# Kernel tuning notes

Measured on AMD Instinct MI355X. Metric: run time of the kernel, lower is better.

## Reference

```python
import jax, jax.numpy as jnp
import numpy as np

N, E, F, S, R, H = 10000, 160000, 128, 10, 8, 64
SH_OFF = [0, 1, 4, 9]
SH_DIM = [1, 3, 5, 7]
AVG_NUM_NEIGHBORS = 16.0


def setup_inputs() -> dict:
    key = jax.random.key(0)
    ks = jax.random.split(key, 16)
    species = jax.random.randint(ks[0], (N,), 0, S)
    node_attrs = jax.nn.one_hot(species, S, dtype=jnp.float32)
    node_feats = jax.random.normal(ks[1], (N, F), dtype=jnp.float32)
    edge_attrs = jax.random.normal(ks[2], (E, 16), dtype=jnp.float32)
    edge_feats = jax.random.normal(ks[3], (E, R), dtype=jnp.float32)
    edge_index = jax.random.randint(ks[4], (2, E), 0, N)
    # learned parameters
    W_skip_node = jax.random.normal(ks[5], (F, S, F), dtype=jnp.float32)
    W_up = jax.random.normal(ks[6], (F, F), dtype=jnp.float32)
    mlp_w1 = jax.random.normal(ks[7], (R, H), dtype=jnp.float32)
    mlp_w2 = jax.random.normal(ks[8], (H, H), dtype=jnp.float32)
    mlp_w3 = jax.random.normal(ks[9], (H, H), dtype=jnp.float32)
    mlp_w4 = jax.random.normal(ks[10], (H, 4 * F), dtype=jnp.float32)  # conv_tp.weight_numel = 512
    W_lin = jax.random.normal(ks[11], (4, F, F), dtype=jnp.float32)
    W_skip_msg = jax.random.normal(ks[12], (4, F, S, F), dtype=jnp.float32)
    W_out = jax.random.normal(ks[13], (F, F), dtype=jnp.float32)
    return dict(node_attrs=node_attrs, node_feats=node_feats, edge_attrs=edge_attrs,
                edge_feats=edge_feats, edge_index=edge_index, species=species,
                W_skip_node=W_skip_node, W_up=W_up, mlp_w1=mlp_w1, mlp_w2=mlp_w2,
                mlp_w3=mlp_w3, mlp_w4=mlp_w4, W_lin=W_lin, W_skip_msg=W_skip_msg,
                W_out=W_out)


def reference(node_attrs, node_feats, edge_attrs, edge_feats, edge_index, species,
              W_skip_node, W_up, mlp_w1, mlp_w2, mlp_w3, mlp_w4,
              W_lin, W_skip_msg, W_out):
    sender, receiver = edge_index[0], edge_index[1]
    num_nodes = node_feats.shape[0]
    num_edges = edge_attrs.shape[0]

    # skip_tp_node: FullyConnectedTensorProduct(128x0e, 10x0e -> 128x0e), fan_in = 128*10
    skip = jnp.einsum('nu,nv,uvw->nw', node_feats, node_attrs, W_skip_node) * (1.0 / np.sqrt(F * S))

    # linear_up: 128x0e -> 128x0e
    h = (node_feats @ W_up) * (1.0 / np.sqrt(F))

    # radial MLP (e3nn FullyConnectedNet: no bias, w/sqrt(fan_in), silu on hidden layers)
    t = edge_feats
    for W in (mlp_w1, mlp_w2, mlp_w3):
        t = jax.nn.silu((t @ W) * (1.0 / np.sqrt(W.shape[0])))
    tp_w = (t @ mlp_w4) * (1.0 / np.sqrt(H))  # [E, 512]

    # conv_tp (gather -> 0e x l -> l 'uvu' TP) fused with scatter_sum per l-block
    hs = h[sender]  # [E, 128]
    msgs = []
    for l in range(4):
        d = SH_DIM[l]
        w_l = tp_w[:, l * F:(l + 1) * F]                       # [E, 128]
        sh_l = edge_attrs[:, SH_OFF[l]:SH_OFF[l] + d]          # [E, d]
        mji = (hs * w_l)[:, :, None] * sh_l[:, None, :]        # [E, 128, d]
        m = jax.ops.segment_sum(mji.reshape(num_edges, F * d), receiver,
                                num_segments=num_nodes)
        msgs.append(m.reshape(num_nodes, F, d))

    inv_avg = 1.0 / np.sqrt(AVG_NUM_NEIGHBORS)
    # linear (per-l 128->128) / sqrt(avg_num_neighbors), then skip_tp_msg (x 10x0e attrs)
    blocks = []
    for l in range(4):
        x = jnp.einsum('num,uw->nwm', msgs[l], W_lin[l]) * (inv_avg / np.sqrt(F))
        x = jnp.einsum('num,nv,uvw->nwm', x, node_attrs, W_skip_msg[l]) * (1.0 / np.sqrt(F * S))
        blocks.append(x)

    # linear_out: target -> 128x0e keeps only the scalar (l=0) block
    message = (blocks[0][:, :, 0] @ W_out) * (1.0 / np.sqrt(F))  # [N, 128]
    return message, skip
```

## Files before the change

kernel.cpp:

```cpp
#include <hip/hip_runtime.h>
#include <math.h>

#define NFEAT 128
#define NSPEC 10

__global__ void k_histboth(const int* __restrict__ species, const int* __restrict__ edge_index,
                           int* __restrict__ counts, int* __restrict__ ehist, int N, int E) {
    int i = blockIdx.x * blockDim.x + threadIdx.x;
    if (i < N) atomicAdd(&counts[species[i]], 1);
    if (i < E) atomicAdd(&ehist[edge_index[E + i]], 1);
}

__global__ void k_build(const int* __restrict__ counts, int* __restrict__ cursor,
                        int4* __restrict__ table, int* __restrict__ nTiles) {
    __shared__ int off[NSPEC + 1], ts[NSPEC + 1], cnt[NSPEC];
    const int t = threadIdx.x;
    if (t == 0) {
        int o = 0, tt = 0;
        for (int s = 0; s < NSPEC; s++) {
            cnt[s] = counts[s];
            off[s] = o; ts[s] = tt;
            o += cnt[s]; tt += (cnt[s] + 63) >> 6;
        }
        off[NSPEC] = o; ts[NSPEC] = tt;
        nTiles[0] = tt;
    }
    __syncthreads();
    if (t < NSPEC) cursor[t] = off[t];
    int nt = ts[NSPEC];
    for (int i = t; i < nt; i += blockDim.x) {
        int s = 0;
        while (ts[s + 1] <= i) s++;
        int b = i - ts[s];
        table[i] = make_int4(s, off[s] + b * 64, min(64, cnt[s] - b * 64), 0);
    }
}

__global__ void k_scatter(const int* __restrict__ species, int* __restrict__ cursor,
                          int* __restrict__ sorted, int N) {
    int i = blockIdx.x * blockDim.x + threadIdx.x;
    if (i < N) {
        int p = atomicAdd(&cursor[species[i]], 1);
        sorted[p] = i;
    }
}

__global__ void k_escan(const int* __restrict__ ehist, int* __restrict__ ecursor, int N) {
    __shared__ int ssum[256];
    const int t = threadIdx.x;
    const int chunk = (N + 255) / 256;
    const int lo = t * chunk;
    const int hi = min(lo + chunk, N);
    int local = 0;
    for (int i = lo; i < hi; i++) local += ehist[i];
    ssum[t] = local;
    __syncthreads();
    for (int off = 1; off < 256; off <<= 1) {
        int x = (t >= off) ? ssum[t - off] : 0;
        __syncthreads();
        ssum[t] += x;
        __syncthreads();
    }
    int run = ssum[t] - local;
    for (int i = lo; i < hi; i++) {
        ecursor[i] = run;
        run += ehist[i];
    }
}

__global__ void k_egather(const int* __restrict__ edge_index, const float* __restrict__ edge_attrs,
                          const float* __restrict__ edge_feats, int* __restrict__ ecursor,
                          int* __restrict__ sendG, int* __restrict__ recvG,
                          float* __restrict__ sh0G, float* __restrict__ efG, int E) {
    int i = blockIdx.x * blockDim.x + threadIdx.x;
    if (i < E) {
        int r = edge_index[E + i];
        int p = atomicAdd(&ecursor[r], 1);
        sendG[p] = edge_index[i];
        recvG[p] = r;
        sh0G[p]  = edge_attrs[(long)i * 16];
        float4 v0 = *(const float4*)(edge_feats + (long)i * 8);
        float4 v1 = *(const float4*)(edge_feats + (long)i * 8 + 4);
        *(float4*)(efG + (long)p * 8)     = v0;
        *(float4*)(efG + (long)p * 8 + 4) = v1;
    }
}

template <int BC>
__global__ __launch_bounds__(256) void k_gemm(
    const float* __restrict__ A, int aStride,
    const float* __restrict__ B, int bStride, int bSpecStride,
    float* __restrict__ C, int cStride, int cChunkY,
    int M, float alpha,
    const int* __restrict__ sorted,
    const int4* __restrict__ table,
    const int* __restrict__ nTiles)
{
    __shared__ float At[128][64];
    __shared__ float Bs[128][BC];
    const int t = threadIdx.x;
    const int gy = blockIdx.y;

    int start, cnt, spec = 0;
    if (table) {
        if (blockIdx.x >= nTiles[0]) return;
        int4 te = table[blockIdx.x];
        spec = te.x; start = te.y; cnt = te.z;
    } else {
        start = blockIdx.x * 64;
        cnt = M - start;
        if (cnt <= 0) return;
        if (cnt > 64) cnt = 64;
    }

    {
        const float* Bp = B + (long)spec * bSpecStride + (long)gy * BC;
        constexpr int F4R = BC / 4;
        #pragma unroll
        for (int i = 0; i < (128 * F4R) / 256; i++) {
            int idx = t + 256 * i;
            int k = idx / F4R;
            int c = (idx % F4R) * 4;
            *(float4*)&Bs[k][c] = *(const float4*)(Bp + (long)k * bStride + c);
        }
    }
    {
        int r = t & 63;
        int kc = (t >> 6) * 32;
        if (r < cnt) {
            int grow = table ? sorted[start + r] : (start + r);
            const float4* src = (const float4*)(A + (long)grow * aStride + kc);
            #pragma unroll
            for (int i = 0; i < 8; i++) {
                float4 v = src[i];
                At[kc + 4*i + 0][r] = v.x;
                At[kc + 4*i + 1][r] = v.y;
                At[kc + 4*i + 2][r] = v.z;
                At[kc + 4*i + 3][r] = v.w;
            }
        } else {
            #pragma unroll
            for (int i = 0; i < 32; i++) At[kc + i][r] = 0.0f;
        }
    }
    __syncthreads();

    constexpr int CG   = BC / 4;
    constexpr int ROWS = BC / 16;
    const int c0 = (t % CG) * 4;
    const int r0 = (t / CG) * ROWS;
    float acc[ROWS][4] = {};
    #pragma unroll 8
    for (int k = 0; k < 128; k++) {
        float4 b = *(const float4*)&Bs[k][c0];
        float av[ROWS];
        #pragma unroll
        for (int i = 0; i < ROWS / 4; i++) {
            float4 a = *(const float4*)&At[k][r0 + 4 * i];
            av[4*i + 0] = a.x; av[4*i + 1] = a.y; av[4*i + 2] = a.z; av[4*i + 3] = a.w;
        }
        #pragma unroll
        for (int i = 0; i < ROWS; i++) {
            acc[i][0] += av[i] * b.x;
            acc[i][1] += av[i] * b.y;
            acc[i][2] += av[i] * b.z;
            acc[i][3] += av[i] * b.w;
        }
    }
    #pragma unroll
    for (int i = 0; i < ROWS; i++) {
        int r = r0 + i;
        if (r < cnt) {
            int grow = table ? sorted[start + r] : (start + r);
            float4 v = make_float4(acc[i][0] * alpha, acc[i][1] * alpha,
                                   acc[i][2] * alpha, acc[i][3] * alpha);
            *(float4*)&C[(long)gy * cChunkY + (long)grow * cStride + c0] = v;
        }
    }
}

__global__ __launch_bounds__(256) void k_hs(
    const float* __restrict__ A,
    const float* __restrict__ Wup,
    const float* __restrict__ Wsn,
    float* __restrict__ h, float* __restrict__ skip,
    const int* __restrict__ sorted, const int4* __restrict__ table,
    const int* __restrict__ nTiles, float aH, float aSkip)
{
    __shared__ float At[128][64];
    __shared__ float Bs[128][64];
    const int t = threadIdx.x;
    const int gy = blockIdx.y;
    if (blockIdx.x >= nTiles[0]) return;
    int4 te = table[blockIdx.x];
    const int spec = te.x, start = te.y, cnt = te.z;

    {
        int r = t & 63, kc = (t >> 6) * 32;
        if (r < cnt) {
            int grow = sorted[start + r];
            const float4* src = (const float4*)(A + (long)grow * NFEAT + kc);
            #pragma unroll
            for (int i = 0; i < 8; i++) {
                float4 v = src[i];
                At[kc + 4*i + 0][r] = v.x;
                At[kc + 4*i + 1][r] = v.y;
                At[kc + 4*i + 2][r] = v.z;
                At[kc + 4*i + 3][r] = v.w;
            }
        } else {
            #pragma unroll
            for (int i = 0; i < 32; i++) At[kc + i][r] = 0.0f;
        }
    }
    const int c0 = (t & 15) * 4;
    const int r0 = (t >> 4) * 4;
    #pragma unroll
    for (int pass = 0; pass < 2; pass++) {
        {
            const float* Bp = pass == 0 ? (Wup + gy * 64)
                                        : (Wsn + spec * NFEAT + gy * 64);
            const int bStride = pass == 0 ? NFEAT : NFEAT * NSPEC;
            #pragma unroll
            for (int i = 0; i < 8; i++) {
                int idx = t + 256 * i;
                int k = idx >> 4;
                int c = (idx & 15) * 4;
                *(float4*)&Bs[k][c] = *(const float4*)(Bp + (long)k * bStride + c);
            }
        }
        __syncthreads();
        float acc[4][4] = {};
        #pragma unroll 8
        for (int k = 0; k < 128; k++) {
            float4 b = *(const float4*)&Bs[k][c0];
            float4 a = *(const float4*)&At[k][r0];
            float av[4] = {a.x, a.y, a.z, a.w};
            #pragma unroll
            for (int i = 0; i < 4; i++) {
                acc[i][0] += av[i] * b.x;
                acc[i][1] += av[i] * b.y;
                acc[i][2] += av[i] * b.z;
                acc[i][3] += av[i] * b.w;
            }
        }
        float* dst   = pass == 0 ? h : skip;
        float  alpha = pass == 0 ? aH : aSkip;
        #pragma unroll
        for (int i = 0; i < 4; i++) {
            int r = r0 + i;
            if (r < cnt) {
                int grow = sorted[start + r];
                float4 v = make_float4(acc[i][0] * alpha, acc[i][1] * alpha,
                                       acc[i][2] * alpha, acc[i][3] * alpha);
                *(float4*)&dst[(long)grow * NFEAT + gy * 64 + c0] = v;
            }
        }
        __syncthreads();
    }
}

#define ASTR 20

__global__ __launch_bounds__(256, 5) void k_edge(
    const int*   __restrict__ sendG,
    const int*   __restrict__ recvG,
    const float* __restrict__ sh0G,
    const float* __restrict__ efG,
    const float* __restrict__ W1,
    const float* __restrict__ W2,
    const float* __restrict__ W3,
    const float* __restrict__ W4,
    const float* __restrict__ h,
    float*       __restrict__ msgs0,
    int E)
{
    __shared__ float W1s[8][64];
    __shared__ float actS[4][64 * ASTR];
    __shared__ float efS[4][8 * 16];
    __shared__ int   sendS[4][16];
    __shared__ int   recvS[4][16];
    __shared__ float sh0S[4][16];

    const int t = threadIdx.x;
    if (t < 128) ((float4*)W1s)[t] = ((const float4*)W1)[t];
    __syncthreads();

    const int wid = t >> 6, lane = t & 63;
    const int ntiles = (E + 15) >> 4;
    const int tile = blockIdx.x * 4 + wid;
    if (tile >= ntiles) return;
    const int base = tile << 4;

    float* act = actS[wid];
    float* ef  = efS[wid];

    {
        int g = lane & 15, p = base + g;
        bool ok = p < E;
        if (lane < 16)      sendS[wid][g] = ok ? sendG[p] : 0;
        else if (lane < 32) recvS[wid][g] = ok ? recvG[p] : -1;
        else if (lane < 48) sh0S[wid][g]  = ok ? sh0G[p]  : 0.0f;
    }
    {
        int idx = lane * 2, e = idx >> 3, k = idx & 7;
        int p = base + e;
        float2 v = make_float2(0.f, 0.f);
        if (p < E) v = *(const float2*)(efG + (long)p * 8 + k);
        ef[k * 16 + e]       = v.x;
        ef[(k + 1) * 16 + e] = v.y;
    }

    const float s1 = 0.3535533905932738f;
    const float s2 = 0.125f;
    const int e4 = lane & 3;
    const int j4 = lane >> 2;

    {
        float acc[4][4] = {};
        #pragma unroll
        for (int k = 0; k < 8; k++) {
            float4 a = *(const float4*)&ef[k * 16 + e4 * 4];
            float4 b = *(const float4*)&W1s[k][j4 * 4];
            float av[4] = {a.x, a.y, a.z, a.w};
            float bv[4] = {b.x, b.y, b.z, b.w};
            #pragma unroll
            for (int jj = 0; jj < 4; jj++)
                #pragma unroll
                for (int ee = 0; ee < 4; ee++)
                    acc[jj][ee] += av[ee] * bv[jj];
        }
        #pragma unroll
        for (int jj = 0; jj < 4; jj++) {
            float4 v; float x;
            x = acc[jj][0] * s1; v.x = x / (1.0f + __expf(-x));
            x = acc[jj][1] * s1; v.y = x / (1.0f + __expf(-x));
            x = acc[jj][2] * s1; v.z = x / (1.0f + __expf(-x));
            x = acc[jj][3] * s1; v.w = x / (1.0f + __expf(-x));
            *(float4*)&act[(j4 * 4 + jj) * ASTR + e4 * 4] = v;
        }
    }

    {
        float acc[4][4] = {};
        const float4* W2v = (const float4*)W2;
        #pragma unroll 4
        for (int k = 0; k < 64; k++) {
            float4 a = *(const float4*)&act[k * ASTR + e4 * 4];
            float4 b = W2v[k * 16 + j4];
            float av[4] = {a.x, a.y, a.z, a.w};
            float bv[4] = {b.x, b.y, b.z, b.w};
            #pragma unroll
            for (int jj = 0; jj < 4; jj++)
                #pragma unroll
                for (int ee = 0; ee < 4; ee++)
                    acc[jj][ee] += av[ee] * bv[jj];
        }
        #pragma unroll
        for (int jj = 0; jj < 4; jj++) {
            float4 v; float x;
            x = acc[jj][0] * s2; v.x = x / (1.0f + __expf(-x));
            x = acc[jj][1] * s2; v.y = x / (1.0f + __expf(-x));
            x = acc[jj][2] * s2; v.z = x / (1.0f + __expf(-x));
            x = acc[jj][3] * s2; v.w = x / (1.0f + __expf(-x));
            *(float4*)&act[(j4 * 4 + jj) * ASTR + e4 * 4] = v;
        }
    }

    {
        float acc[4][4] = {};
        const float4* W3v = (const float4*)W3;
        #pragma unroll 4
        for (int k = 0; k < 64; k++) {
            float4 a = *(const float4*)&act[k * ASTR + e4 * 4];
            float4 b = W3v[k * 16 + j4];
            float av[4] = {a.x, a.y, a.z, a.w};
            float bv[4] = {b.x, b.y, b.z, b.w};
            #pragma unroll
            for (int jj = 0; jj < 4; jj++)
                #pragma unroll
                for (int ee = 0; ee < 4; ee++)
                    acc[jj][ee] += av[ee] * bv[jj];
        }
        #pragma unroll
        for (int jj = 0; jj < 4; jj++) {
            float4 v; float x;
            x = acc[jj][0] * s2; v.x = x / (1.0f + __expf(-x));
            x = acc[jj][1] * s2; v.y = x / (1.0f + __expf(-x));
            x = acc[jj][2] * s2; v.z = x / (1.0f + __expf(-x));
            x = acc[jj][3] * s2; v.w = x / (1.0f + __expf(-x));
            *(float4*)&act[(j4 * 4 + jj) * ASTR + e4 * 4] = v;
        }
    }

    {
        const int c0 = lane * 2;
        float wacc[16][2] = {};
        #pragma unroll 4
        for (int k = 0; k < 64; k++) {
            float2 w4 = *(const float2*)&W4[k * 512 + c0];
            float4 a0 = *(const float4*)&act[k * ASTR + 0];
            float4 a1 = *(const float4*)&act[k * ASTR + 4];
            float4 a2 = *(const float4*)&act[k * ASTR + 8];
            float4 a3 = *(const float4*)&act[k * ASTR + 12];
            float av[16] = {a0.x, a0.y, a0.z, a0.w, a1.x, a1.y, a1.z, a1.w,
                            a2.x, a2.y, a2.z, a2.w, a3.x, a3.y, a3.z, a3.w};
            #pragma unroll
            for (int e = 0; e < 16; e++) {
                wacc[e][0] += av[e] * w4.x;
                wacc[e][1] += av[e] * w4.y;
            }
        }
        int cur = recvS[wid][0];
        float sum0 = 0.f, sum1 = 0.f;
        #pragma unroll
        for (int e = 0; e < 16; e++) {
            int rcv = recvS[wid][e];
            if (rcv != cur) {
                if (cur >= 0) {
                    atomicAdd(&msgs0[(long)cur * NFEAT + c0],     sum0);
                    atomicAdd(&msgs0[(long)cur * NFEAT + c0 + 1], sum1);
                }
                cur = rcv; sum0 = 0.f; sum1 = 0.f;
            }
            float f = sh0S[wid][e] * s2;
            int snd = sendS[wid][e];
            float2 hv = *(const float2*)&h[(long)snd * NFEAT + c0];
            sum0 += wacc[e][0] * f * hv.x;
            sum1 += wacc[e][1] * f * hv.y;
        }
        if (cur >= 0) {
            atomicAdd(&msgs0[(long)cur * NFEAT + c0],     sum0);
            atomicAdd(&msgs0[(long)cur * NFEAT + c0 + 1], sum1);
        }
    }
}

extern "C" void kernel_launch(void* const* d_in, const int* in_sizes, int n_in,
                              void* d_out, int out_size, void* d_ws, size_t ws_size,
                              hipStream_t stream) {
    const float* node_feats = (const float*)d_in[1];
    const float* edge_attrs = (const float*)d_in[2];
    const float* edge_feats = (const float*)d_in[3];
    const int*   edge_index = (const int*)  d_in[4];
    const int*   species    = (const int*)  d_in[5];
    const float* Wsn        = (const float*)d_in[6];
    const float* Wup        = (const float*)d_in[7];
    const float* W1         = (const float*)d_in[8];
    const float* W2         = (const float*)d_in[9];
    const float* W3         = (const float*)d_in[10];
    const float* W4         = (const float*)d_in[11];
    const float* Wlin       = (const float*)d_in[12];
    const float* Wsm        = (const float*)d_in[13];
    const float* Wout       = (const float*)d_in[14];

    const int N = in_sizes[5];
    const int E = in_sizes[4] / 2;
    const int NF = NFEAT;

    float* out     = (float*)d_out;
    float* message = out;
    float* skip    = out + (long)N * NF;

    char* wsb = (char*)d_ws;
    size_t off = 0;
    auto carve = [&](size_t bytes) { void* p = wsb + off; off = (off + bytes + 255) & ~(size_t)255; return p; };
    float* h      = (float*)carve((size_t)N * NF * 4);
    float* msgs0  = (float*)carve((size_t)N * NF * 4);
    float* Tst    = (float*)carve((size_t)NSPEC * NF * NF * 4);
    float* Comb   = (float*)carve((size_t)NSPEC * NF * NF * 4);
    int*   sorted = (int*)carve((size_t)N * 4);
    int*   counts = (int*)carve(64);
    int*   cursor = (int*)carve(64);
    int*   nTiles = (int*)carve(16);
    int4*  table  = (int4*)carve(256 * 16);
    int*   ehist  = (int*)carve((size_t)N * 4);
    int*   ecursor= (int*)carve((size_t)N * 4);
    int*   sendG  = (int*)carve((size_t)E * 4);
    int*   recvG  = (int*)carve((size_t)E * 4);
    float* sh0G   = (float*)carve((size_t)E * 4);
    float* efG    = (float*)carve((size_t)E * 8 * 4);

    const float aH    = 1.0f / sqrtf((float)NF);
    const float aSkip = 1.0f / sqrtf((float)(NF * NSPEC));
    const float cTot  = 0.25f / ((float)NF * sqrtf((float)(NF * NSPEC)));

    hipMemsetAsync(counts, 0, 64, stream);
    hipMemsetAsync(ehist, 0, (size_t)N * 4, stream);
    hipMemsetAsync(msgs0, 0, (size_t)N * NF * 4, stream);

    k_histboth<<<(max(N, E) + 255) / 256, 256, 0, stream>>>(species, edge_index, counts, ehist, N, E);
    k_build  <<<1, 256, 0, stream>>>(counts, cursor, table, nTiles);
    k_scatter<<<(N + 255) / 256, 256, 0, stream>>>(species, cursor, sorted, N);
    k_escan  <<<1, 256, 0, stream>>>(ehist, ecursor, N);
    k_egather<<<(E + 255) / 256, 256, 0, stream>>>(edge_index, edge_attrs, edge_feats,
                                                   ecursor, sendG, recvG, sh0G, efG, E);

    const int mTiles   = (N + 63) / 64;
    const int maxTiles = mTiles + NSPEC;

    k_hs<<<dim3(maxTiles, 2), 256, 0, stream>>>(
        node_feats, Wup, Wsn, h, skip, sorted, table, nTiles, aH, aSkip);

    k_gemm<128><<<dim3(2, NSPEC), 256, 0, stream>>>(
        Wlin, NF, Wsm, NF * NSPEC, 0, Tst, NF, NF * NF, NF, 1.0f, nullptr, nullptr, nullptr);

    k_gemm<128><<<dim3((NSPEC * NF) / 64, 1), 256, 0, stream>>>(
        Tst, NF, Wout, NF, 0, Comb, NF, NF, NSPEC * NF, cTot, nullptr, nullptr, nullptr);

    int eTiles = (E + 15) / 16;
    int eBlocks = (eTiles + 3) / 4;
    k_edge<<<eBlocks, 256, 0, stream>>>(
        sendG, recvG, sh0G, efG, W1, W2, W3, W4, h, msgs0, E);

    k_gemm<64><<<dim3(maxTiles, 2), 256, 0, stream>>>(
        msgs0, NF, Comb, NF, NF * NF, message, NF, 64, N, 1.0f, sorted, table, nTiles);
}
```

Baseline: 362.9 us.

## Compute radial MLP per edge in registers with one thread per edge

The edge kernel is restructured so each thread owns one edge and runs the whole radial MLP in registers. Weight reads are wave-uniform, so they can become scalar loads, which removes the shared-memory activation tiles and the cross-lane GEMM tiling. Blocks shrink to a single 64-lane wave covering 64 edges. The gather/scatter phase now stages the 128 used TP weights through shared memory in four 32-column chunks, with 32 lanes walking edges serially. This trades high register pressure and a half-idle, longer serial scatter loop for cheaper MLP arithmetic.

```diff
diff --git a/kernel.cpp b/kernel.cpp
--- a/kernel.cpp
+++ b/kernel.cpp
@@ -260,9 +260,7 @@
     }
 }
 
-#define ASTR 20
-
-__global__ __launch_bounds__(256, 5) void k_edge(
+__global__ __launch_bounds__(64, 3) void k_edge(
     const int*   __restrict__ sendG,
     const int*   __restrict__ recvG,
     const float* __restrict__ sh0G,
@@ -275,163 +273,124 @@
     float*       __restrict__ msgs0,
     int E)
 {
-    __shared__ float W1s[8][64];
-    __shared__ float actS[4][64 * ASTR];
-    __shared__ float efS[4][8 * 16];
-    __shared__ int   sendS[4][16];
-    __shared__ int   recvS[4][16];
-    __shared__ float sh0S[4][16];
-
-    const int t = threadIdx.x;
-    if (t < 128) ((float4*)W1s)[t] = ((const float4*)W1)[t];
-    __syncthreads();
-
-    const int wid = t >> 6, lane = t & 63;
-    const int ntiles = (E + 15) >> 4;
-    const int tile = blockIdx.x * 4 + wid;
-    if (tile >= ntiles) return;
-    const int base = tile << 4;
-
-    float* act = actS[wid];
-    float* ef  = efS[wid];
+    __shared__ float act2w[64 * 36];
+    __shared__ int   sendS[64];
+    __shared__ int   recvS[64];
+    __shared__ float sh0S[64];
+
+    const int lane = threadIdx.x;
+    const long base = (long)blockIdx.x * 64;
+    const int nE = (E - (int)base < 64) ? (E - (int)base) : 64;
 
     {
-        int g = lane & 15, p = base + g;
-        bool ok = p < E;
-        if (lane < 16)      sendS[wid][g] = ok ? sendG[p] : 0;
-        else if (lane < 32) recvS[wid][g] = ok ? recvG[p] : -1;
-        else if (lane < 48) sh0S[wid][g]  = ok ? sh0G[p]  : 0.0f;
-    }
-    {
-        int idx = lane * 2, e = idx >> 3, k = idx & 7;
-        int p = base + e;
-        float2 v = make_float2(0.f, 0.f);
-        if (p < E) v = *(const float2*)(efG + (long)p * 8 + k);
-        ef[k * 16 + e]       = v.x;
-        ef[(k + 1) * 16 + e] = v.y;
+        int p = (int)base + lane;
+        bool ok = lane < nE;
+        sendS[lane] = ok ? sendG[p] : 0;
+        recvS[lane] = ok ? recvG[p] : -1;
+        sh0S[lane]  = ok ? sh0G[p]  : 0.0f;
+    }
+
+    float ef[8];
+    if (lane < nE) {
+        float4 v0 = *(const float4*)(efG + (base + lane) * 8);
+        float4 v1 = *(const float4*)(efG + (base + lane) * 8 + 4);
+        ef[0] = v0.x; ef[1] = v0.y; ef[2] = v0.z; ef[3] = v0.w;
+        ef[4] = v1.x; ef[5] = v1.y; ef[6] = v1.z; ef[7] = v1.w;
+    } else {
+        #pragma unroll
+        for (int k = 0; k < 8; k++) ef[k] = 0.0f;
     }
 
     const float s1 = 0.3535533905932738f;
     const float s2 = 0.125f;
-    const int e4 = lane & 3;
-    const int j4 = lane >> 2;
-
-    {
-        float acc[4][4] = {};
+
+    float ta[64], tb[64];
+
+    #pragma unroll
+    for (int jc = 0; jc < 4; jc++) {
+        float acc[16];
+        #pragma unroll
+        for (int u = 0; u < 16; u++) acc[u] = 0.0f;
         #pragma unroll
         for (int k = 0; k < 8; k++) {
-            float4 a = *(const float4*)&ef[k * 16 + e4 * 4];
-            float4 b = *(const float4*)&W1s[k][j4 * 4];
-            float av[4] = {a.x, a.y, a.z, a.w};
-            float bv[4] = {b.x, b.y, b.z, b.w};
-            #pragma unroll
-            for (int jj = 0; jj < 4; jj++)
-                #pragma unroll
-                for (int ee = 0; ee < 4; ee++)
-                    acc[jj][ee] += av[ee] * bv[jj];
-        }
-        #pragma unroll
-        for (int jj = 0; jj < 4; jj++) {
-            float4 v; float x;
-            x = acc[jj][0] * s1; v.x = x / (1.0f + __expf(-x));
-            x = acc[jj][1] * s1; v.y = x / (1.0f + __expf(-x));
-            x = acc[jj][2] * s1; v.z = x / (1.0f + __expf(-x));
-            x = acc[jj][3] * s1; v.w = x / (1.0f + __expf(-x));
-            *(float4*)&act[(j4 * 4 + jj) * ASTR + e4 * 4] = v;
-        }
-    }
-
-    {
-        float acc[4][4] = {};
-        const float4* W2v = (const float4*)W2;
-        #pragma unroll 4
+            #pragma unroll
+            for (int u = 0; u < 16; u++)
+                acc[u] += ef[k] * W1[k * 64 + jc * 16 + u];
+        }
+        #pragma unroll
+        for (int u = 0; u < 16; u++) {
+            float x = acc[u] * s1;
+            ta[jc * 16 + u] = x / (1.0f + __expf(-x));
+        }
+    }
+
+    #pragma unroll
+    for (int jc = 0; jc < 4; jc++) {
+        float acc[16];
+        #pragma unroll
+        for (int u = 0; u < 16; u++) acc[u] = 0.0f;
+        #pragma unroll
         for (int k = 0; k < 64; k++) {
-            float4 a = *(const float4*)&act[k * ASTR + e4 * 4];
-            float4 b = W2v[k * 16 + j4];
-            float av[4] = {a.x, a.y, a.z, a.w};
-            float bv[4] = {b.x, b.y, b.z, b.w};
-            #pragma unroll
-            for (int jj = 0; jj < 4; jj++)
-                #pragma unroll
-                for (int ee = 0; ee < 4; ee++)
-                    acc[jj][ee] += av[ee] * bv[jj];
-        }
-        #pragma unroll
-        for (int jj = 0; jj < 4; jj++) {
-            float4 v; float x;
-            x = acc[jj][0] * s2; v.x = x / (1.0f + __expf(-x));
-            x = acc[jj][1] * s2; v.y = x / (1.0f + __expf(-x));
-            x = acc[jj][2] * s2; v.z = x / (1.0f + __expf(-x));
-            x = acc[jj][3] * s2; v.w = x / (1.0f + __expf(-x));
-            *(float4*)&act[(j4 * 4 + jj) * ASTR + e4 * 4] = v;
-        }
-    }
-
-    {
-        float acc[4][4] = {};
-        const float4* W3v = (const float4*)W3;
-        #pragma unroll 4
+            #pragma unroll
+            for (int u = 0; u < 16; u++)
+                acc[u] += ta[k] * W2[k * 64 + jc * 16 + u];
+        }
+        #pragma unroll
+        for (int u = 0; u < 16; u++) {
+            float x = acc[u] * s2;
+            tb[jc * 16 + u] = x / (1.0f + __expf(-x));
+        }
+    }
+
+    #pragma unroll
+    for (int jc = 0; jc < 4; jc++) {
+        float acc[16];
+        #pragma unroll
+        for (int u = 0; u < 16; u++) acc[u] = 0.0f;
+        #pragma unroll
         for (int k = 0; k < 64; k++) {
-            float4 a = *(const float4*)&act[k * ASTR + e4 * 4];
-            float4 b = W3v[k * 16 + j4];
-            float av[4] = {a.x, a.y, a.z, a.w};
-            float bv[4] = {b.x, b.y, b.z, b.w};
-            #pragma unroll
-            for (int jj = 0; jj < 4; jj++)
-                #pragma unroll
-                for (int ee = 0; ee < 4; ee++)
-                    acc[jj][ee] += av[ee] * bv[jj];
-        }
-        #pragma unroll
-        for (int jj = 0; jj < 4; jj++) {
-            float4 v; float x;
-            x = acc[jj][0] * s2; v.x = x / (1.0f + __expf(-x));
-            x = acc[jj][1] * s2; v.y = x / (1.0f + __expf(-x));
-            x = acc[jj][2] * s2; v.z = x / (1.0f + __expf(-x));
-            x = acc[jj][3] * s2; v.w = x / (1.0f + __expf(-x));
-            *(float4*)&act[(j4 * 4 + jj) * ASTR + e4 * 4] = v;
-        }
-    }
-
-    {
-        const int c0 = lane * 2;
-        float wacc[16][2] = {};
-        #pragma unroll 4
+            #pragma unroll
+            for (int u = 0; u < 16; u++)
+                acc[u] += tb[k] * W3[k * 64 + jc * 16 + u];
+        }
+        #pragma unroll
+        for (int u = 0; u < 16; u++) {
+            float x = acc[u] * s2;
+            ta[jc * 16 + u] = x / (1.0f + __expf(-x));
+        }
+    }
+
+    for (int ch = 0; ch < 4; ch++) {
+        float out[32];
+        #pragma unroll
+        for (int u = 0; u < 32; u++) out[u] = 0.0f;
+        #pragma unroll
         for (int k = 0; k < 64; k++) {
-            float2 w4 = *(const float2*)&W4[k * 512 + c0];
-            float4 a0 = *(const float4*)&act[k * ASTR + 0];
-            float4 a1 = *(const float4*)&act[k * ASTR + 4];
-            float4 a2 = *(const float4*)&act[k * ASTR + 8];
-            float4 a3 = *(const float4*)&act[k * ASTR + 12];
-            float av[16] = {a0.x, a0.y, a0.z, a0.w, a1.x, a1.y, a1.z, a1.w,
-                            a2.x, a2.y, a2.z, a2.w, a3.x, a3.y, a3.z, a3.w};
-            #pragma unroll
-            for (int e = 0; e < 16; e++) {
-                wacc[e][0] += av[e] * w4.x;
-                wacc[e][1] += av[e] * w4.y;
-            }
-        }
-        int cur = recvS[wid][0];
-        float sum0 = 0.f, sum1 = 0.f;
-        #pragma unroll
-        for (int e = 0; e < 16; e++) {
-            int rcv = recvS[wid][e];
-            if (rcv != cur) {
-                if (cur >= 0) {
-                    atomicAdd(&msgs0[(long)cur * NFEAT + c0],     sum0);
-                    atomicAdd(&msgs0[(long)cur * NFEAT + c0 + 1], sum1);
+            #pragma unroll
+            for (int u = 0; u < 32; u++)
+                out[u] += ta[k] * W4[k * 512 + ch * 32 + u];
+        }
+        #pragma unroll
+        for (int u = 0; u < 32; u += 4)
+            *(float4*)&act2w[lane * 36 + u] =
+                make_float4(out[u], out[u + 1], out[u + 2], out[u + 3]);
+        if (lane < 32) {
+            int cur = -1;
+            float sum = 0.0f;
+            for (int e = 0; e < nE; e++) {
+                int rcv = recvS[e];
+                if (rcv != cur) {
+                    if (cur >= 0)
+                        atomicAdd(&msgs0[(long)cur * NFEAT + ch * 32 + lane], sum);
+                    cur = rcv; sum = 0.0f;
                 }
-                cur = rcv; sum0 = 0.f; sum1 = 0.f;
-            }
-            float f = sh0S[wid][e] * s2;
-            int snd = sendS[wid][e];
-            float2 hv = *(const float2*)&h[(long)snd * NFEAT + c0];
-            sum0 += wacc[e][0] * f * hv.x;
-            sum1 += wacc[e][1] * f * hv.y;
-        }
-        if (cur >= 0) {
-            atomicAdd(&msgs0[(long)cur * NFEAT + c0],     sum0);
-            atomicAdd(&msgs0[(long)cur * NFEAT + c0 + 1], sum1);
+                float f = sh0S[e] * s2;
+                int snd = sendS[e];
+                float hv = h[(long)snd * NFEAT + ch * 32 + lane];
+                sum += act2w[e * 36 + lane] * f * hv;
+            }
+            if (cur >= 0)
+                atomicAdd(&msgs0[(long)cur * NFEAT + ch * 32 + lane], sum);
         }
     }
 }
@@ -508,9 +467,8 @@
     k_gemm<128><<<dim3((NSPEC * NF) / 64, 1), 256, 0, stream>>>(
         Tst, NF, Wout, NF, 0, Comb, NF, NF, NSPEC * NF, cTot, nullptr, nullptr, nullptr);
 
-    int eTiles = (E + 15) / 16;
-    int eBlocks = (eTiles + 3) / 4;
-    k_edge<<<eBlocks, 256, 0, stream>>>(
+    int eBlocks = (E + 63) / 64;
+    k_edge<<<eBlocks, 64, 0, stream>>>(
         sendG, recvG, sh0G, efG, W1, W2, W3, W4, h, msgs0, E);
 
     k_gemm<64><<<dim3(maxTiles, 2), 256, 0, stream>>>(
```

Result: slower. 1.183 ms (+226.1%).
